# Kernel optimization log

Hardware: AMD Instinct MI355X
Metric: run time of the kernel (lower is better)

Reference implementation:

```python
import jax, jax.numpy as jnp
import numpy as np

BIT_WIDTH = 1
LEVELS = 2 ** BIT_WIDTH - 1
# Floyd-Steinberg gather weights (mirrored scatter kernel): contributions to
# pixel (r,c) from (r-1,c-1), (r-1,c), (r-1,c+1), (r,c-1)
W_UL, W_U, W_UR, W_L = 1.0 / 16, 5.0 / 16, 3.0 / 16, 7.0 / 16


def quant(x):
    return jnp.round(x * LEVELS) / LEVELS


def dither(x01):
    """Raster-scan error-diffusion dithering. x01: [B,C,R,W] in [0,1]."""
    B, C, R, W = x01.shape
    dtype = x01.dtype

    def row_step(prev_err, row_x):
        # prev_err: [B,C,W+2] zero-padded errors of previous row
        # row_x:    [W,B,C]   input values of current row
        up = (W_UL * prev_err[..., 0:W]
              + W_U * prev_err[..., 1:W + 1]
              + W_UR * prev_err[..., 2:W + 2])          # [B,C,W]
        up = jnp.moveaxis(up, -1, 0)                     # [W,B,C]

        def col_step(left_err, xs):
            x, u = xs                                    # each [B,C]
            val = jnp.clip(x + u + W_L * left_err, 0.0, 1.0)
            err = val - quant(val)
            return err, (val, err)

        _, (vals, errs) = jax.lax.scan(col_step, jnp.zeros((B, C), dtype), (row_x, up))
        err_row = jnp.pad(jnp.moveaxis(errs, 0, -1), ((0, 0), (0, 0), (1, 1)))  # [B,C,W+2]
        return err_row, jnp.moveaxis(vals, 0, -1)        # carry, [B,C,W]

    rows_x = jnp.moveaxis(jnp.moveaxis(x01, 2, 0), -1, 1)  # [R,W,B,C]
    init = jnp.zeros((B, C, W + 2), dtype)
    _, out_rows = jax.lax.scan(row_step, init, rows_x)      # [R,B,C,W]
    out = jnp.moveaxis(out_rows, 0, 2)                      # [B,C,R,W]
    return quant(out)


def setup_inputs() -> dict:
    key = jax.random.key(0)
    x = jax.random.normal(key, (32, 3, 512, 512), dtype=jnp.float32)
    return {"x": x}


def reference(x):
    x = jnp.clip(x, -1.0, 1.0)
    x01 = (x + 1.0) / 2.0
    y = dither(x01)
    return y * 2.0 - 1.0
```

## Files before the change

### kernel.cpp

```cpp
#include <hip/hip_runtime.h>


#define F_UL 0.0625f
#define F_U  0.3125f
#define F_UR 0.1875f
#define F_L  0.4375f

typedef unsigned long long ull;

constexpr int WW    = 512;
constexpr int IMG   = WW * WW;
constexpr int NIMG  = 96;
constexpr int NW    = 8;
constexpr int BUFW  = 792;
constexpr int NCH   = 40;
constexpr int LAG   = 10;
constexpr int PPAIR = 320;
constexpr size_t XP_FLOATS = (size_t)NIMG * NW * PPAIR * 128;
constexpr size_t XP_BYTES  = XP_FLOATS * 4;
constexpr size_t XP_SLACK  = 8192;
constexpr size_t XP_OFF    = 4u * 1024 * 1024;
constexpr size_t WS_NEED   = XP_OFF + XP_BYTES + XP_SLACK;

__device__ __forceinline__ float wave_shr1(float v, float fill) {
  int r = __builtin_amdgcn_update_dpp(__float_as_int(fill), __float_as_int(v),
                                      0x138 , 0xF, 0xF, false);
  return __int_as_float(r);
}

__device__ __forceinline__ float pp(float xv) {
#pragma clang fp contract(off)
  float xc = fminf(fmaxf(xv, -1.0f), 1.0f);
  return (xc + 1.0f) * 0.5f;
}

__global__ __launch_bounds__(512)
void pack_kernel(const float* __restrict__ xin, float* __restrict__ xp) {
  __shared__ float ring[4 * 4160];
  const int img = blockIdx.x, w = blockIdx.y;
  const int tid = threadIdx.x;
  const int wv  = tid >> 6, l = tid & 63;

  const float* xg = xin + (size_t)img * IMG + (size_t)w * 64 * WW;
  float* ob = xp + ((size_t)(img * NW + w) * PPAIR) * 128;

  float4 rv[2];
  auto issue_tile = [&](int t) {
    const float* src = xg + 64 * t;
#pragma unroll
    for (int k = 0; k < 2; ++k) {
      int flat = tid + 512 * k;
      int row = flat >> 4, cq = flat & 15;
      rv[k] = *(const float4*)(src + row * WW + cq * 4);
    }
  };
  auto write_tile = [&](int t) {
    float* dst = ring + (t & 3) * 4160;
#pragma unroll
    for (int k = 0; k < 2; ++k) {
      int flat = tid + 512 * k;
      int row = flat >> 4, cq = flat & 15;
      float* d = dst + row * 65 + cq * 4;
      d[0] = pp(rv[k].x); d[1] = pp(rv[k].y);
      d[2] = pp(rv[k].z); d[3] = pp(rv[k].w);
    }
  };

  issue_tile(0);
  write_tile(0);
  __syncthreads();
  for (int t = 0; t < 10; ++t) {
    if (t < 7) issue_tile(t + 1);
    const int Mb = 32 * t + 4 * wv;
#pragma unroll
    for (int i = 0; i < 4; ++i) {
      const int M  = Mb + i;
      const int g  = 2 * (M - l);
      const int gm = g & 511;
      const int idx = ((gm >> 6) & 3) * 4160 + l * 65 + (gm & 63);
      const bool ok = ((unsigned)g < 512u);
      float va = ring[idx], vb = ring[idx + 1];
      float2 v = make_float2(ok ? va : -8.0f, ok ? vb : -8.0f);
      *(float2*)(ob + (size_t)M * 128 + 2 * l) = v;
    }
    if (t < 7) write_tile(t + 1);
    __syncthreads();
  }
}

__global__ __launch_bounds__(512, 1)
void dither_packed(const float* __restrict__ xp, float* __restrict__ yout) {
  __shared__ float bnd[(NW + 1) * BUFW];
  __shared__ int   flags[NW];
  __shared__ ull   bits[NW][11][65];
  __shared__ float4 lut4[16];

  const int  tid  = threadIdx.x;
  const int  wave = tid >> 6;
  const int  lane = tid & 63;
  const int  img  = blockIdx.x;
  const bool l63  = (lane == 63);

  for (int i = tid; i < (NW + 1) * BUFW; i += 512) bnd[i] = 0.0f;
  if (tid < NW) flags[tid] = 0;
  if (tid < 16)
    lut4[tid] = make_float4((tid & 1) ? 1.0f : -1.0f, (tid & 2) ? 1.0f : -1.0f,
                            (tid & 4) ? 1.0f : -1.0f, (tid & 8) ? 1.0f : -1.0f);
  bits[wave][10][lane] = 0ull;
  __syncthreads();

  const float* xw = xp + ((size_t)(img * NW + wave) * PPAIR) * 128 + lane * 2;
  float* bufR = bnd + wave * BUFW;
  float* bufW = bnd + (wave + 1) * BUFW;

  float2 X0[4], X1[4], X2[4], X3[4], X4[4], X5[4], X6[4], X7[4];
#pragma unroll
  for (int i = 0; i < 4; ++i) {
    X0[i] = *(const float2*)(xw + (size_t)(0  + i) * 128);
    X1[i] = *(const float2*)(xw + (size_t)(4  + i) * 128);
    X2[i] = *(const float2*)(xw + (size_t)(8  + i) * 128);
    X3[i] = *(const float2*)(xw + (size_t)(12 + i) * 128);
  }

  int seen = 0;
  if (wave) {
    while ((seen = __hip_atomic_load(&flags[wave - 1], __ATOMIC_RELAXED,
                                     __HIP_MEMORY_SCOPE_WORKGROUP)) < LAG)
      __builtin_amdgcn_s_sleep(1);
    __asm__ volatile("s_waitcnt lgkmcnt(0)" ::: "memory");
  }

  float err = 0.0f, s2 = 0.0f;
  float s1 = (lane == 0) ? bufR[129] : 0.0f;
  float2 Q0[4], Q1[4];
#pragma unroll
  for (int i = 0; i < 4; ++i) {
    Q0[i] = *(const float2*)(bufR + 130 + 2 * i);
    Q1[i] = *(const float2*)(bufR + 138 + 2 * i);
  }

  float accA = 0.0f, accB = 0.0f, accC = 0.0f;

  auto step = [&](float qv, float xv) -> float {
#pragma clang fp contract(off)
    float e_in = wave_shr1(err, qv);
    float t1   = F_UL * s2;
    float t2   = F_U  * s1;
    float t3   = F_UR * e_in;
    float u    = (t1 + t2) + t3;
    float a1   = xv + u;
    float b    = F_L * err;
    float v    = a1 + b;
    float val  = __builtin_amdgcn_fmed3f(v, 0.0f, 1.0f);
    float qn   = rintf(val);
    err = val - qn;
    s2 = s1; s1 = e_in;
    return qn;
  };

  auto iter8 = [&](float2 (&XC)[4], float2 (&XL)[4], float2 (&QC)[4],
                   int T, float& acc, float W) {
    const float* lp = xw + (size_t)(T / 2 + 16) * 128;
    XL[0] = *(const float2*)(lp + 0 * 128);
    XL[1] = *(const float2*)(lp + 1 * 128);
    XL[2] = *(const float2*)(lp + 2 * 128);
    XL[3] = *(const float2*)(lp + 3 * 128);

    float p0 = step(QC[0].x, XC[0].x); float e0 = err;
    float p1 = step(QC[0].y, XC[0].y); float e1 = err;
    float p2 = step(QC[1].x, XC[1].x); float e2 = err;
    float p3 = step(QC[1].y, XC[1].y); float e3 = err;
    float p4 = step(QC[2].x, XC[2].x); float e4 = err;
    float p5 = step(QC[2].y, XC[2].y); float e5 = err;
    float p6 = step(QC[3].x, XC[3].x); float e6 = err;
    float p7 = step(QC[3].y, XC[3].y); float e7 = err;

    QC[0] = *(const float2*)(bufR + (T + 146));
    QC[1] = *(const float2*)(bufR + (T + 148));
    QC[2] = *(const float2*)(bufR + (T + 150));
    QC[3] = *(const float2*)(bufR + (T + 152));

    {
#pragma clang fp contract(off)
      acc += p0 * (W * 1.0f);
      acc += p1 * (W * 2.0f);
      acc += p2 * (W * 4.0f);
      acc += p3 * (W * 8.0f);
      acc += p4 * (W * 16.0f);
      acc += p5 * (W * 32.0f);
      acc += p6 * (W * 64.0f);
      acc += p7 * (W * 128.0f);
    }

    if (l63) {
      float* bw = bufW + (T + 3);
      bw[0] = e0; bw[1] = e1; bw[2] = e2; bw[3] = e3;
      bw[4] = e4; bw[5] = e5; bw[6] = e6; bw[7] = e7;
    }
  };

  auto waitflag = [&](int j) {
    if (wave) {
      int need = j + LAG; if (need > NCH) need = NCH;
      if (seen < need) {
        while ((seen = __hip_atomic_load(&flags[wave - 1], __ATOMIC_RELAXED,
                                         __HIP_MEMORY_SCOPE_WORKGROUP)) < need)
          __builtin_amdgcn_s_sleep(1);
        __asm__ volatile("s_waitcnt lgkmcnt(0)" ::: "memory");
      }
    }
  };
  auto pubflag = [&](int v) {
    if (l63) {
      __asm__ volatile("s_waitcnt lgkmcnt(0)" ::: "memory");
      __hip_atomic_store(&flags[wave], v, __ATOMIC_RELAXED,
                         __HIP_MEMORY_SCOPE_WORKGROUP);
    }
  };

  for (int jj = 0; jj < NCH; jj += 4) {
    const int T0 = 16 * jj;
    waitflag(jj);
    iter8(X0, X4, Q0, T0 + 0,  accA, 1.0f);
    iter8(X1, X5, Q1, T0 + 8,  accA, 256.0f);
    pubflag(jj + 1);
    waitflag(jj + 1);
    iter8(X2, X6, Q0, T0 + 16, accA, 65536.0f);
    iter8(X3, X7, Q1, T0 + 24, accB, 1.0f);
    pubflag(jj + 2);
    waitflag(jj + 2);
    iter8(X4, X0, Q0, T0 + 32, accB, 256.0f);
    iter8(X5, X1, Q1, T0 + 40, accB, 65536.0f);
    pubflag(jj + 3);
    waitflag(jj + 3);
    iter8(X6, X2, Q0, T0 + 48, accC, 1.0f);
    iter8(X7, X3, Q1, T0 + 56, accC, 256.0f);
    pubflag(jj + 4);
    unsigned u0 = (unsigned)accA;
    unsigned u1 = (unsigned)accB;
    unsigned u2 = (unsigned)accC;
    unsigned lo = u0 | (u1 << 24);
    unsigned hi = (u1 >> 8) | (u2 << 16);
    *(uint2*)&bits[wave][jj >> 2][lane] = make_uint2(lo, hi);
    accA = 0.0f; accB = 0.0f; accC = 0.0f;
  }

  float* ybase = yout + (size_t)img * IMG + (size_t)(wave * 64) * WW + 8 * lane;
  for (int rr = 0; rr < 64; ++rr) {
    const int t0 = 8 * lane + 2 * rr;
    const int t64 = t0 >> 6, sh = t0 & 63;
    ull w1 = bits[wave][t64][rr];
    ull w2 = bits[wave][t64 + 1][rr];
    unsigned b = (unsigned)((w1 >> sh) | ((w2 << 1) << (63 - sh)));
    float* orow = ybase + (size_t)rr * WW;
    *(float4*)(orow)     = lut4[b & 15u];
    *(float4*)(orow + 4) = lut4[(b >> 4) & 15u];
  }
}

__global__ __launch_bounds__(512, 1)
void dither_direct(const float* __restrict__ xin, float* __restrict__ yout) {
  __shared__ float bnd[(NW + 1) * BUFW];
  __shared__ int flags[NW];

  const int  tid  = threadIdx.x;
  const int  wave = tid >> 6;
  const int  lane = tid & 63;
  const int  img  = blockIdx.x;
  const bool l63  = (lane == 63);

  for (int i = tid; i < (NW + 1) * BUFW; i += 512) bnd[i] = 0.0f;
  if (tid < NW) flags[tid] = 0;
  __syncthreads();

  const int r = wave * 64 + lane;
  const float* xrow = xin + (size_t)img * IMG + (size_t)r * WW;
  float*       yrow = yout + (size_t)img * IMG + (size_t)r * WW;
  float* bufR = bnd + wave * BUFW;
  float* bufW = bnd + (wave + 1) * BUFW;
  const int c0 = -2 * lane;

  auto ldx = [&](int c) -> float2 { return *(const float2*)(xrow + (c & 511)); };

  float2 A0 = ldx(c0 + 0),  A1 = ldx(c0 + 2),  A2 = ldx(c0 + 4),  A3 = ldx(c0 + 6);
  float2 pB0 = ldx(c0 + 8),  pB1 = ldx(c0 + 10), pB2 = ldx(c0 + 12), pB3 = ldx(c0 + 14);
  float2 pC0 = ldx(c0 + 16), pC1 = ldx(c0 + 18), pC2 = ldx(c0 + 20), pC3 = ldx(c0 + 22);
  float xq0 = pp(A0.x), xq1 = pp(A0.y), xq2 = pp(A1.x), xq3 = pp(A1.y);
  float xq4 = pp(A2.x), xq5 = pp(A2.y), xq6 = pp(A3.x), xq7 = pp(A3.y);
  float2 pA0 = pB0, pA1 = pB1, pA2 = pB2, pA3 = pB3;
  pB0 = pC0; pB1 = pC1; pB2 = pC2; pB3 = pC3;

  if (wave) {
    while (__hip_atomic_load(&flags[wave - 1], __ATOMIC_RELAXED,
                             __HIP_MEMORY_SCOPE_WORKGROUP) < LAG)
      __builtin_amdgcn_s_sleep(1);
    __asm__ volatile("s_waitcnt lgkmcnt(0)" ::: "memory");
  }

  float err = 0.0f, s2 = 0.0f;
  float s1 = (lane == 0) ? bufR[129] : 0.0f;
  float2 qa = *(const float2*)(bufR + 130);
  float2 qb = *(const float2*)(bufR + 132);
  float2 qc = *(const float2*)(bufR + 134);
  float2 qd = *(const float2*)(bufR + 136);
  float2 fa = *(const float2*)(bufR + 138);
  float2 fb = *(const float2*)(bufR + 140);
  float2 fc = *(const float2*)(bufR + 142);
  float2 fd = *(const float2*)(bufR + 144);

  auto step = [&](int c, float qv, float xv) -> float {
#pragma clang fp contract(off)
    float e_in = wave_shr1(err, qv);
    float t1   = F_UL * s2;
    float t2   = F_U  * s1;
    float t3   = F_UR * e_in;
    float u    = (t1 + t2) + t3;
    float a1   = xv + u;
    float b    = F_L * err;
    float v    = a1 + b;
    float val  = fminf(fmaxf(v, 0.0f), 1.0f);
    float qn   = rintf(val);
    float e    = val - qn;
    float en   = ((unsigned)c < 512u) ? e : 0.0f;
    err = en; s2 = s1; s1 = e_in;
    return __builtin_fmaf(qn, 2.0f, -1.0f);
  };

  auto iter8 = [&](int T) {
    const int cg = c0 + T;
    float2 n0 = ldx(cg + 24), n1 = ldx(cg + 26), n2 = ldx(cg + 28), n3 = ldx(cg + 30);
    float2 h0 = *(const float2*)(bufR + (T + 146));
    float2 h1 = *(const float2*)(bufR + (T + 148));
    float2 h2 = *(const float2*)(bufR + (T + 150));
    float2 h3 = *(const float2*)(bufR + (T + 152));
    float w0 = pp(pA0.x), w1 = pp(pA0.y), w2 = pp(pA1.x), w3 = pp(pA1.y);
    float w4 = pp(pA2.x), w5 = pp(pA2.y), w6 = pp(pA3.x), w7 = pp(pA3.y);

    float y0 = step(cg + 0, qa.x, xq0); float e0 = err;
    float y1 = step(cg + 1, qa.y, xq1); float e1 = err;
    float y2 = step(cg + 2, qb.x, xq2); float e2 = err;
    float y3 = step(cg + 3, qb.y, xq3); float e3 = err;
    float y4 = step(cg + 4, qc.x, xq4); float e4 = err;
    float y5 = step(cg + 5, qc.y, xq5); float e5 = err;
    float y6 = step(cg + 6, qd.x, xq6); float e6 = err;
    float y7 = step(cg + 7, qd.y, xq7); float e7 = err;

    if ((unsigned)(cg + 0) < 511u) *(float2*)(yrow + cg + 0) = make_float2(y0, y1);
    if ((unsigned)(cg + 2) < 511u) *(float2*)(yrow + cg + 2) = make_float2(y2, y3);
    if ((unsigned)(cg + 4) < 511u) *(float2*)(yrow + cg + 4) = make_float2(y4, y5);
    if ((unsigned)(cg + 6) < 511u) *(float2*)(yrow + cg + 6) = make_float2(y6, y7);

    if (l63) {
      float* bw = bufW + (cg + 129);
      bw[0] = e0; bw[1] = e1; bw[2] = e2; bw[3] = e3;
      bw[4] = e4; bw[5] = e5; bw[6] = e6; bw[7] = e7;
    }

    xq0 = w0; xq1 = w1; xq2 = w2; xq3 = w3;
    xq4 = w4; xq5 = w5; xq6 = w6; xq7 = w7;
    pA0 = pB0; pA1 = pB1; pA2 = pB2; pA3 = pB3;
    pB0 = n0;  pB1 = n1;  pB2 = n2;  pB3 = n3;
    qa = fa; qb = fb; qc = fc; qd = fd;
    fa = h0; fb = h1; fc = h2; fd = h3;
  };

  for (int j = 0; j < NCH; ++j) {
    if (wave) {
      int need = j + LAG; if (need > NCH) need = NCH;
      while (__hip_atomic_load(&flags[wave - 1], __ATOMIC_RELAXED,
                               __HIP_MEMORY_SCOPE_WORKGROUP) < need)
        __builtin_amdgcn_s_sleep(1);
      __asm__ volatile("s_waitcnt lgkmcnt(0)" ::: "memory");
    }
    iter8(16 * j);
    iter8(16 * j + 8);
    if (l63) {
      __asm__ volatile("s_waitcnt lgkmcnt(0)" ::: "memory");
      __hip_atomic_store(&flags[wave], j + 1, __ATOMIC_RELAXED,
                         __HIP_MEMORY_SCOPE_WORKGROUP);
    }
  }
}

extern "C" void kernel_launch(void* const* d_in, const int* in_sizes, int n_in,
                              void* d_out, int out_size, void* d_ws, size_t ws_size,
                              hipStream_t stream) {
  const float* x = (const float*)d_in[0];
  float*       y = (float*)d_out;
  if (ws_size >= WS_NEED) {
    float* xp = (float*)((char*)d_ws + XP_OFF);
    pack_kernel<<<dim3(NIMG, NW), dim3(512), 0, stream>>>(x, xp);
    dither_packed<<<dim3(NIMG), dim3(512), 0, stream>>>(xp, y);
  } else {
    dither_direct<<<dim3(NIMG), dim3(512), 0, stream>>>(x, y);
  }
}
```

Measured before the change: 279.4 us.

## Interleave two images per workgroup to hide serial dependency latency

Each workgroup now processes two independent image channels at once, interleaving their error-diffusion steps so that each image's dependent chain (cross-lane shift, arithmetic, rounding) can overlap with the other's. Shared-memory boundary buffers and bit arrays are duplicated, and the grid is halved to 48 blocks. This increases ILP inside the latency-bound scan at the cost of more registers and LDS, and uses fewer workgroups than the 256 CUs available.

New measurement: 362.9 us. 1.3x slower.

```diff
diff --git a/kernel.cpp b/kernel.cpp
--- a/kernel.cpp
+++ b/kernel.cpp
@@ -89,37 +89,48 @@
 }
 
 __global__ __launch_bounds__(512, 1)
-void dither_packed(const float* __restrict__ xp, float* __restrict__ yout) {
-  __shared__ float bnd[(NW + 1) * BUFW];
+void dither_packed2(const float* __restrict__ xp, float* __restrict__ yout) {
+  __shared__ float bndA[(NW + 1) * BUFW];
+  __shared__ float bndB[(NW + 1) * BUFW];
   __shared__ int   flags[NW];
-  __shared__ ull   bits[NW][11][65];
+  __shared__ ull   bitsA[NW][11][65];
+  __shared__ ull   bitsB[NW][11][65];
   __shared__ float4 lut4[16];
 
   const int  tid  = threadIdx.x;
   const int  wave = tid >> 6;
   const int  lane = tid & 63;
-  const int  img  = blockIdx.x;
+  const int  imgA = 2 * blockIdx.x;
   const bool l63  = (lane == 63);
 
-  for (int i = tid; i < (NW + 1) * BUFW; i += 512) bnd[i] = 0.0f;
+  for (int i = tid; i < (NW + 1) * BUFW; i += 512) { bndA[i] = 0.0f; bndB[i] = 0.0f; }
   if (tid < NW) flags[tid] = 0;
   if (tid < 16)
     lut4[tid] = make_float4((tid & 1) ? 1.0f : -1.0f, (tid & 2) ? 1.0f : -1.0f,
                             (tid & 4) ? 1.0f : -1.0f, (tid & 8) ? 1.0f : -1.0f);
-  bits[wave][10][lane] = 0ull;
+  bitsA[wave][10][lane] = 0ull;
+  bitsB[wave][10][lane] = 0ull;
   __syncthreads();
 
-  const float* xw = xp + ((size_t)(img * NW + wave) * PPAIR) * 128 + lane * 2;
-  float* bufR = bnd + wave * BUFW;
-  float* bufW = bnd + (wave + 1) * BUFW;
-
-  float2 X0[4], X1[4], X2[4], X3[4], X4[4], X5[4], X6[4], X7[4];
+  const float* xwA = xp + ((size_t)(imgA * NW + wave) * PPAIR) * 128 + lane * 2;
+  const float* xwB = xp + ((size_t)((imgA + 1) * NW + wave) * PPAIR) * 128 + lane * 2;
+  float* bufRA = bndA + wave * BUFW;
+  float* bufWA = bndA + (wave + 1) * BUFW;
+  float* bufRB = bndB + wave * BUFW;
+  float* bufWB = bndB + (wave + 1) * BUFW;
+
+  float2 XA0[4], XA1[4], XA2[4], XA3[4], XA4[4], XA5[4], XA6[4], XA7[4];
+  float2 XB0[4], XB1[4], XB2[4], XB3[4], XB4[4], XB5[4], XB6[4], XB7[4];
 #pragma unroll
   for (int i = 0; i < 4; ++i) {
-    X0[i] = *(const float2*)(xw + (size_t)(0  + i) * 128);
-    X1[i] = *(const float2*)(xw + (size_t)(4  + i) * 128);
-    X2[i] = *(const float2*)(xw + (size_t)(8  + i) * 128);
-    X3[i] = *(const float2*)(xw + (size_t)(12 + i) * 128);
+    XA0[i] = *(const float2*)(xwA + (size_t)(0  + i) * 128);
+    XB0[i] = *(const float2*)(xwB + (size_t)(0  + i) * 128);
+    XA1[i] = *(const float2*)(xwA + (size_t)(4  + i) * 128);
+    XB1[i] = *(const float2*)(xwB + (size_t)(4  + i) * 128);
+    XA2[i] = *(const float2*)(xwA + (size_t)(8  + i) * 128);
+    XB2[i] = *(const float2*)(xwB + (size_t)(8  + i) * 128);
+    XA3[i] = *(const float2*)(xwA + (size_t)(12 + i) * 128);
+    XB3[i] = *(const float2*)(xwB + (size_t)(12 + i) * 128);
   }
 
   int seen = 0;
@@ -130,72 +141,112 @@
     __asm__ volatile("s_waitcnt lgkmcnt(0)" ::: "memory");
   }
 
-  float err = 0.0f, s2 = 0.0f;
-  float s1 = (lane == 0) ? bufR[129] : 0.0f;
-  float2 Q0[4], Q1[4];
+  float errA = 0.0f, s2A = 0.0f, s1A = (lane == 0) ? bufRA[129] : 0.0f;
+  float errB = 0.0f, s2B = 0.0f, s1B = (lane == 0) ? bufRB[129] : 0.0f;
+  float2 QA0[4], QA1[4], QB0[4], QB1[4];
 #pragma unroll
   for (int i = 0; i < 4; ++i) {
-    Q0[i] = *(const float2*)(bufR + 130 + 2 * i);
-    Q1[i] = *(const float2*)(bufR + 138 + 2 * i);
-  }
-
-  float accA = 0.0f, accB = 0.0f, accC = 0.0f;
-
-  auto step = [&](float qv, float xv) -> float {
+    QA0[i] = *(const float2*)(bufRA + 130 + 2 * i);
+    QA1[i] = *(const float2*)(bufRA + 138 + 2 * i);
+    QB0[i] = *(const float2*)(bufRB + 130 + 2 * i);
+    QB1[i] = *(const float2*)(bufRB + 138 + 2 * i);
+  }
+
+  float aA0 = 0.0f, aA1 = 0.0f, aA2 = 0.0f;
+  float aB0 = 0.0f, aB1 = 0.0f, aB2 = 0.0f;
+
+  auto stepA = [&](float qv, float xv) -> float {
 #pragma clang fp contract(off)
-    float e_in = wave_shr1(err, qv);
-    float t1   = F_UL * s2;
-    float t2   = F_U  * s1;
+    float e_in = wave_shr1(errA, qv);
+    float t1   = F_UL * s2A;
+    float t2   = F_U  * s1A;
     float t3   = F_UR * e_in;
     float u    = (t1 + t2) + t3;
     float a1   = xv + u;
-    float b    = F_L * err;
+    float b    = F_L * errA;
     float v    = a1 + b;
     float val  = __builtin_amdgcn_fmed3f(v, 0.0f, 1.0f);
     float qn   = rintf(val);
-    err = val - qn;
-    s2 = s1; s1 = e_in;
+    errA = val - qn;
+    s2A = s1A; s1A = e_in;
     return qn;
   };
-
-  auto iter8 = [&](float2 (&XC)[4], float2 (&XL)[4], float2 (&QC)[4],
-                   int T, float& acc, float W) {
-    const float* lp = xw + (size_t)(T / 2 + 16) * 128;
-    XL[0] = *(const float2*)(lp + 0 * 128);
-    XL[1] = *(const float2*)(lp + 1 * 128);
-    XL[2] = *(const float2*)(lp + 2 * 128);
-    XL[3] = *(const float2*)(lp + 3 * 128);
-
-    float p0 = step(QC[0].x, XC[0].x); float e0 = err;
-    float p1 = step(QC[0].y, XC[0].y); float e1 = err;
-    float p2 = step(QC[1].x, XC[1].x); float e2 = err;
-    float p3 = step(QC[1].y, XC[1].y); float e3 = err;
-    float p4 = step(QC[2].x, XC[2].x); float e4 = err;
-    float p5 = step(QC[2].y, XC[2].y); float e5 = err;
-    float p6 = step(QC[3].x, XC[3].x); float e6 = err;
-    float p7 = step(QC[3].y, XC[3].y); float e7 = err;
-
-    QC[0] = *(const float2*)(bufR + (T + 146));
-    QC[1] = *(const float2*)(bufR + (T + 148));
-    QC[2] = *(const float2*)(bufR + (T + 150));
-    QC[3] = *(const float2*)(bufR + (T + 152));
+  auto stepB = [&](float qv, float xv) -> float {
+#pragma clang fp contract(off)
+    float e_in = wave_shr1(errB, qv);
+    float t1   = F_UL * s2B;
+    float t2   = F_U  * s1B;
+    float t3   = F_UR * e_in;
+    float u    = (t1 + t2) + t3;
+    float a1   = xv + u;
+    float b    = F_L * errB;
+    float v    = a1 + b;
+    float val  = __builtin_amdgcn_fmed3f(v, 0.0f, 1.0f);
+    float qn   = rintf(val);
+    errB = val - qn;
+    s2B = s1B; s1B = e_in;
+    return qn;
+  };
+
+  auto iter8_2 = [&](float2 (&XCa)[4], float2 (&XLa)[4], float2 (&QCa)[4],
+                     float2 (&XCb)[4], float2 (&XLb)[4], float2 (&QCb)[4],
+                     int T, float& acca, float& accb, float W) {
+    const float* lpA = xwA + (size_t)(T / 2 + 16) * 128;
+    const float* lpB = xwB + (size_t)(T / 2 + 16) * 128;
+    XLa[0] = *(const float2*)(lpA + 0 * 128);
+    XLb[0] = *(const float2*)(lpB + 0 * 128);
+    XLa[1] = *(const float2*)(lpA + 1 * 128);
+    XLb[1] = *(const float2*)(lpB + 1 * 128);
+    XLa[2] = *(const float2*)(lpA + 2 * 128);
+    XLb[2] = *(const float2*)(lpB + 2 * 128);
+    XLa[3] = *(const float2*)(lpA + 3 * 128);
+    XLb[3] = *(const float2*)(lpB + 3 * 128);
+
+    float pA0 = stepA(QCa[0].x, XCa[0].x); float eA0 = errA;
+    float pB0 = stepB(QCb[0].x, XCb[0].x); float eB0 = errB;
+    float pA1 = stepA(QCa[0].y, XCa[0].y); float eA1 = errA;
+    float pB1 = stepB(QCb[0].y, XCb[0].y); float eB1 = errB;
+    float pA2 = stepA(QCa[1].x, XCa[1].x); float eA2 = errA;
+    float pB2 = stepB(QCb[1].x, XCb[1].x); float eB2 = errB;
+    float pA3 = stepA(QCa[1].y, XCa[1].y); float eA3 = errA;
+    float pB3 = stepB(QCb[1].y, XCb[1].y); float eB3 = errB;
+    float pA4 = stepA(QCa[2].x, XCa[2].x); float eA4 = errA;
+    float pB4 = stepB(QCb[2].x, XCb[2].x); float eB4 = errB;
+    float pA5 = stepA(QCa[2].y, XCa[2].y); float eA5 = errA;
+    float pB5 = stepB(QCb[2].y, XCb[2].y); float eB5 = errB;
+    float pA6 = stepA(QCa[3].x, XCa[3].x); float eA6 = errA;
+    float pB6 = stepB(QCb[3].x, XCb[3].x); float eB6 = errB;
+    float pA7 = stepA(QCa[3].y, XCa[3].y); float eA7 = errA;
+    float pB7 = stepB(QCb[3].y, XCb[3].y); float eB7 = errB;
+
+    QCa[0] = *(const float2*)(bufRA + (T + 146));
+    QCb[0] = *(const float2*)(bufRB + (T + 146));
+    QCa[1] = *(const float2*)(bufRA + (T + 148));
+    QCb[1] = *(const float2*)(bufRB + (T + 148));
+    QCa[2] = *(const float2*)(bufRA + (T + 150));
+    QCb[2] = *(const float2*)(bufRB + (T + 150));
+    QCa[3] = *(const float2*)(bufRA + (T + 152));
+    QCb[3] = *(const float2*)(bufRB + (T + 152));
 
     {
 #pragma clang fp contract(off)
-      acc += p0 * (W * 1.0f);
-      acc += p1 * (W * 2.0f);
-      acc += p2 * (W * 4.0f);
-      acc += p3 * (W * 8.0f);
-      acc += p4 * (W * 16.0f);
-      acc += p5 * (W * 32.0f);
-      acc += p6 * (W * 64.0f);
-      acc += p7 * (W * 128.0f);
+      acca += pA0 * (W * 1.0f);   accb += pB0 * (W * 1.0f);
+      acca += pA1 * (W * 2.0f);   accb += pB1 * (W * 2.0f);
+      acca += pA2 * (W * 4.0f);   accb += pB2 * (W * 4.0f);
+      acca += pA3 * (W * 8.0f);   accb += pB3 * (W * 8.0f);
+      acca += pA4 * (W * 16.0f);  accb += pB4 * (W * 16.0f);
+      acca += pA5 * (W * 32.0f);  accb += pB5 * (W * 32.0f);
+      acca += pA6 * (W * 64.0f);  accb += pB6 * (W * 64.0f);
+      acca += pA7 * (W * 128.0f); accb += pB7 * (W * 128.0f);
     }
 
     if (l63) {
-      float* bw = bufW + (T + 3);
-      bw[0] = e0; bw[1] = e1; bw[2] = e2; bw[3] = e3;
-      bw[4] = e4; bw[5] = e5; bw[6] = e6; bw[7] = e7;
+      float* bwA = bufWA + (T + 3);
+      bwA[0] = eA0; bwA[1] = eA1; bwA[2] = eA2; bwA[3] = eA3;
+      bwA[4] = eA4; bwA[5] = eA5; bwA[6] = eA6; bwA[7] = eA7;
+      float* bwB = bufWB + (T + 3);
+      bwB[0] = eB0; bwB[1] = eB1; bwB[2] = eB2; bwB[3] = eB3;
+      bwB[4] = eB4; bwB[5] = eB5; bwB[6] = eB6; bwB[7] = eB7;
     }
   };
 
@@ -221,40 +272,47 @@
   for (int jj = 0; jj < NCH; jj += 4) {
     const int T0 = 16 * jj;
     waitflag(jj);
-    iter8(X0, X4, Q0, T0 + 0,  accA, 1.0f);
-    iter8(X1, X5, Q1, T0 + 8,  accA, 256.0f);
+    iter8_2(XA0, XA4, QA0, XB0, XB4, QB0, T0 + 0,  aA0, aB0, 1.0f);
+    iter8_2(XA1, XA5, QA1, XB1, XB5, QB1, T0 + 8,  aA0, aB0, 256.0f);
     pubflag(jj + 1);
     waitflag(jj + 1);
-    iter8(X2, X6, Q0, T0 + 16, accA, 65536.0f);
-    iter8(X3, X7, Q1, T0 + 24, accB, 1.0f);
+    iter8_2(XA2, XA6, QA0, XB2, XB6, QB0, T0 + 16, aA0, aB0, 65536.0f);
+    iter8_2(XA3, XA7, QA1, XB3, XB7, QB1, T0 + 24, aA1, aB1, 1.0f);
     pubflag(jj + 2);
     waitflag(jj + 2);
-    iter8(X4, X0, Q0, T0 + 32, accB, 256.0f);
-    iter8(X5, X1, Q1, T0 + 40, accB, 65536.0f);
+    iter8_2(XA4, XA0, QA0, XB4, XB0, QB0, T0 + 32, aA1, aB1, 256.0f);
+    iter8_2(XA5, XA1, QA1, XB5, XB1, QB1, T0 + 40, aA1, aB1, 65536.0f);
     pubflag(jj + 3);
     waitflag(jj + 3);
-    iter8(X6, X2, Q0, T0 + 48, accC, 1.0f);
-    iter8(X7, X3, Q1, T0 + 56, accC, 256.0f);
+    iter8_2(XA6, XA2, QA0, XB6, XB2, QB0, T0 + 48, aA2, aB2, 1.0f);
+    iter8_2(XA7, XA3, QA1, XB7, XB3, QB1, T0 + 56, aA2, aB2, 256.0f);
     pubflag(jj + 4);
-    unsigned u0 = (unsigned)accA;
-    unsigned u1 = (unsigned)accB;
-    unsigned u2 = (unsigned)accC;
-    unsigned lo = u0 | (u1 << 24);
-    unsigned hi = (u1 >> 8) | (u2 << 16);
-    *(uint2*)&bits[wave][jj >> 2][lane] = make_uint2(lo, hi);
-    accA = 0.0f; accB = 0.0f; accC = 0.0f;
-  }
-
-  float* ybase = yout + (size_t)img * IMG + (size_t)(wave * 64) * WW + 8 * lane;
-  for (int rr = 0; rr < 64; ++rr) {
-    const int t0 = 8 * lane + 2 * rr;
-    const int t64 = t0 >> 6, sh = t0 & 63;
-    ull w1 = bits[wave][t64][rr];
-    ull w2 = bits[wave][t64 + 1][rr];
-    unsigned b = (unsigned)((w1 >> sh) | ((w2 << 1) << (63 - sh)));
-    float* orow = ybase + (size_t)rr * WW;
-    *(float4*)(orow)     = lut4[b & 15u];
-    *(float4*)(orow + 4) = lut4[(b >> 4) & 15u];
+    {
+      unsigned u0 = (unsigned)aA0, u1 = (unsigned)aA1, u2 = (unsigned)aA2;
+      *(uint2*)&bitsA[wave][jj >> 2][lane] =
+          make_uint2(u0 | (u1 << 24), (u1 >> 8) | (u2 << 16));
+      unsigned v0 = (unsigned)aB0, v1 = (unsigned)aB1, v2 = (unsigned)aB2;
+      *(uint2*)&bitsB[wave][jj >> 2][lane] =
+          make_uint2(v0 | (v1 << 24), (v1 >> 8) | (v2 << 16));
+      aA0 = aA1 = aA2 = 0.0f;
+      aB0 = aB1 = aB2 = 0.0f;
+    }
+  }
+
+  for (int im = 0; im < 2; ++im) {
+    const ull (*bits)[11][65] = im ? bitsB : bitsA;
+    float* ybase = yout + (size_t)(imgA + im) * IMG +
+                   (size_t)(wave * 64) * WW + 8 * lane;
+    for (int rr = 0; rr < 64; ++rr) {
+      const int t0 = 8 * lane + 2 * rr;
+      const int t64 = t0 >> 6, sh = t0 & 63;
+      ull w1 = bits[wave][t64][rr];
+      ull w2 = bits[wave][t64 + 1][rr];
+      unsigned b = (unsigned)((w1 >> sh) | ((w2 << 1) << (63 - sh)));
+      float* orow = ybase + (size_t)rr * WW;
+      *(float4*)(orow)     = lut4[b & 15u];
+      *(float4*)(orow + 4) = lut4[(b >> 4) & 15u];
+    }
   }
 }
 
@@ -390,7 +448,7 @@
   if (ws_size >= WS_NEED) {
     float* xp = (float*)((char*)d_ws + XP_OFF);
     pack_kernel<<<dim3(NIMG, NW), dim3(512), 0, stream>>>(x, xp);
-    dither_packed<<<dim3(NIMG), dim3(512), 0, stream>>>(xp, y);
+    dither_packed2<<<dim3(NIMG / 2), dim3(512), 0, stream>>>(xp, y);
   } else {
     dither_direct<<<dim3(NIMG), dim3(512), 0, stream>>>(x, y);
   }
```
